# Kernel tuning notes

Measured on AMD Instinct MI355X. Metric: run time of the kernel, lower is better.

The kernel has to match this reference:

```python
import jax, jax.numpy as jnp
import numpy as np

B, S, D, E, TOPK = 8, 4096, 1024, 64, 2
TEMP = 0.01


def setup_inputs() -> dict:
    key = jax.random.key(0)
    k_x, k_w1, k_b1, k_w2, k_b2 = jax.random.split(key, 5)
    x = jax.random.normal(k_x, (B, S, D), dtype=jnp.float32)
    # torch.nn.Linear default init ~ U(-1/sqrt(fan_in), 1/sqrt(fan_in)); scale ok for reference
    W1 = jax.random.normal(k_w1, (D, 2 * D), dtype=jnp.float32) * (1.0 / np.sqrt(D))
    b1 = jax.random.normal(k_b1, (2 * D,), dtype=jnp.float32) * 0.01
    W2 = jax.random.normal(k_w2, (2 * D, E), dtype=jnp.float32) * (1.0 / np.sqrt(2 * D))
    b2 = jax.random.normal(k_b2, (E,), dtype=jnp.float32) * 0.01
    return {"x": x, "W1": W1, "b1": b1, "W2": W2, "b2": b2}


def reference(x, W1, b1, W2, b2):
    # 2-layer MLP router: [B,S,D] -> [B,S,2D] -> [B,S,E]
    h = jax.nn.relu(jnp.einsum('bsd,df->bsf', x, W1) + b1)
    logits = jnp.einsum('bsf,fe->bse', h, W2) + b2
    # top-k over experts
    top_k_logits, indices = jax.lax.top_k(logits, TOPK)  # [B,S,K]
    # scatter top-k logits into a -inf-filled tensor: equivalent to masking,
    # since scattered values equal logits at those positions
    keep = jax.nn.one_hot(indices, E, dtype=bool).any(axis=-2)  # [B,S,E]
    sparse_logits = jnp.where(keep, logits, -jnp.inf)
    router_output = jax.nn.softmax(sparse_logits, axis=-1)
    ori_router_output = jax.nn.softmax(logits / TEMP, axis=-1)
    return (ori_router_output, router_output, indices)
```

## Files before the change

### kernel.cpp

```cpp
#include <hip/hip_runtime.h>
#include <math.h>
#include <stdint.h>

#define M_TOK 32768
#define D_IN  1024
#define F_HID 2048
#define E_EXP 64

#define O_ORI 0
#define O_RTR (M_TOK * E_EXP)
#define O_IDX (2 * M_TOK * E_EXP)

typedef _Float16 half8 __attribute__((ext_vector_type(8)));
typedef float    f32x4 __attribute__((ext_vector_type(4)));
typedef unsigned int uint32;
typedef uint32   u32x4 __attribute__((ext_vector_type(4)));

#define WS_XH  ((size_t)0)
#define WS_XL  (WS_XH  + (size_t)M_TOK * D_IN * 2)
#define WS_W1H (WS_XL  + (size_t)M_TOK * D_IN * 2)
#define WS_W1L (WS_W1H + (size_t)D_IN * F_HID * 2)
#define WS_W2H (WS_W1L + (size_t)D_IN * F_HID * 2)
#define WS_W2L (WS_W2H + (size_t)F_HID * E_EXP * 2)
#define WS_H   (WS_W2L + (size_t)F_HID * E_EXP * 2)
#define WS_NEED_SPLIT (WS_H)
#define WS_NEED_FULL  (WS_H + (size_t)M_TOK * F_HID * 4)

__device__ __forceinline__ void split_sc(float v, float sc, unsigned short& h, unsigned short& l) {
    const _Float16 hh = (_Float16)v;
    const float hf = (float)hh;
    const _Float16 hs = (_Float16)(hf * sc);
    const _Float16 ls = (_Float16)((v - hf) * sc);
    h = __builtin_bit_cast(unsigned short, hs);
    l = __builtin_bit_cast(unsigned short, ls);
}


__global__ void split_x_k(const float* __restrict__ x,
                          unsigned short* __restrict__ xh, unsigned short* __restrict__ xl) {
    size_t i = ((size_t)blockIdx.x * 256 + threadIdx.x) * 4;
    const float4 v = *(const float4*)&x[i];
    ushort4 h, l;
    split_sc(v.x, 64.f, h.x, l.x); split_sc(v.y, 64.f, h.y, l.y);
    split_sc(v.z, 64.f, h.z, l.z); split_sc(v.w, 64.f, h.w, l.w);
    *(ushort4*)&xh[i] = h;
    *(ushort4*)&xl[i] = l;
}

__global__ void split_w1t_k(const float* __restrict__ W1,
                            unsigned short* __restrict__ wh, unsigned short* __restrict__ wl) {
    __shared__ float t[32][33];
    const int d0 = blockIdx.x * 32;
    const int f0 = blockIdx.y * 32;
    const int r  = threadIdx.x >> 3;
    const int c4 = (threadIdx.x & 7) * 4;
    const float4 v = *(const float4*)&W1[(size_t)(d0 + r) * F_HID + f0 + c4];
    t[r][c4 + 0] = v.x; t[r][c4 + 1] = v.y; t[r][c4 + 2] = v.z; t[r][c4 + 3] = v.w;
    __syncthreads();
    ushort4 h, l;
    split_sc(t[c4 + 0][r], 64.f, h.x, l.x);
    split_sc(t[c4 + 1][r], 64.f, h.y, l.y);
    split_sc(t[c4 + 2][r], 64.f, h.z, l.z);
    split_sc(t[c4 + 3][r], 64.f, h.w, l.w);
    *(ushort4*)&wh[(size_t)(f0 + r) * D_IN + d0 + c4] = h;
    *(ushort4*)&wl[(size_t)(f0 + r) * D_IN + d0 + c4] = l;
}

__global__ void split_w2t_k(const float* __restrict__ W2,
                            unsigned short* __restrict__ wh, unsigned short* __restrict__ wl) {
    const int gid = blockIdx.x * 256 + threadIdx.x;
    const int e  = gid >> 9;
    const int f4 = (gid & 511) * 4;
    ushort4 h, l;
    split_sc(W2[(size_t)(f4 + 0) * E_EXP + e], 16.f, h.x, l.x);
    split_sc(W2[(size_t)(f4 + 1) * E_EXP + e], 16.f, h.y, l.y);
    split_sc(W2[(size_t)(f4 + 2) * E_EXP + e], 16.f, h.z, l.z);
    split_sc(W2[(size_t)(f4 + 3) * E_EXP + e], 16.f, h.w, l.w);
    *(ushort4*)&wh[(size_t)e * F_HID + f4] = h;
    *(ushort4*)&wl[(size_t)e * F_HID + f4] = l;
}


__device__ __forceinline__ uint32 swz(uint32 o) { return o ^ (((o >> 7) & 7u) << 4); }

#define STAGE16(SRCP, DSTP) \
    __builtin_amdgcn_global_load_lds((const __attribute__((address_space(1))) void*)(SRCP), \
                                     (__attribute__((address_space(3))) void*)(DSTP), 16, 0, 0)


__launch_bounds__(512, 2)
__global__ void gemm1_8w(const unsigned short* __restrict__ xh, const unsigned short* __restrict__ xl,
                         const unsigned short* __restrict__ w1h, const unsigned short* __restrict__ w1l,
                         const float* __restrict__ b1,
                         uint32* __restrict__ hout)
{
    __shared__ __align__(16) unsigned char As[2][32768];
    __shared__ __align__(16) unsigned char Bs[2][32768];

    const int tid  = threadIdx.x;
    const int lane = tid & 63;
    const int w    = tid >> 6;
    const int c15  = lane & 15;
    const int g    = lane >> 4;
    const int wr   = w >> 2;
    const int wc   = w & 3;

    const int bid  = blockIdx.x;
    const int fblk = bid & 7;
    const int mblk = bid >> 3;
    const size_t tok0 = (size_t)mblk * 256;
    const int f0 = fblk * 256;

    uint32 srow[2], shalf[2];
#pragma unroll
    for (int j = 0; j < 2; ++j) {
        const uint32 c_ = (uint32)(w + 8 * j);
        const uint32 s_ = swz(c_ * 1024u + (uint32)lane * 16u);
        srow[j] = s_ >> 6; shalf[j] = (s_ & 63u) >> 1;
    }

    uint32 offA[8], offB[4];
#pragma unroll
    for (int m = 0; m < 8; ++m)
        offA[m] = swz((uint32)(wr * 128 + m * 16 + c15) * 64u + (uint32)g * 16u);
#pragma unroll
    for (int n = 0; n < 4; ++n)
        offB[n] = swz((uint32)(wc * 64 + n * 16 + c15) * 64u + (uint32)g * 16u);

    f32x4 acc[8][4];
#pragma unroll
    for (int m = 0; m < 8; ++m)
#pragma unroll
        for (int n = 0; n < 4; ++n) acc[m][n] = (f32x4){0.f, 0.f, 0.f, 0.f};

#define STAGE_T(T, BUF) do {                                                        \
    const int d0_ = (T) * 32;                                                       \
    _Pragma("unroll")                                                               \
    for (int j = 0; j < 2; ++j) {                                                   \
        const uint32 c_ = (uint32)(w + 8 * j);                                      \
        const size_t asrc = (tok0 + srow[j]) * D_IN + (size_t)(d0_ + (int)shalf[j]);\
        const size_t bsrc = ((size_t)(f0) + srow[j]) * D_IN + (size_t)(d0_ + (int)shalf[j]); \
        STAGE16(xh  + asrc, &As[BUF][c_ * 1024]);                                   \
        STAGE16(xl  + asrc, &As[BUF][16384 + c_ * 1024]);                           \
        STAGE16(w1h + bsrc, &Bs[BUF][c_ * 1024]);                                   \
        STAGE16(w1l + bsrc, &Bs[BUF][16384 + c_ * 1024]);                           \
    } } while (0)

    STAGE_T(0, 0);
    STAGE_T(1, 1);

#pragma unroll 1
    for (int t = 0; t < 32; ++t) {
        if (t < 31) asm volatile("s_waitcnt vmcnt(8)" ::: "memory");
        else        asm volatile("s_waitcnt vmcnt(0)" ::: "memory");
        __builtin_amdgcn_s_barrier();
        const unsigned char* Ab = As[t & 1];
        const unsigned char* Bb = Bs[t & 1];

        half8 b1f[4], b2f[4];
#pragma unroll
        for (int n = 0; n < 4; ++n) {
            b1f[n] = *(const half8*)(Bb + offB[n]);
            b2f[n] = *(const half8*)(Bb + 16384 + offB[n]);
        }
        half8 a1f[4], a2f[4];
#pragma unroll
        for (int m = 0; m < 4; ++m) {
            a1f[m] = *(const half8*)(Ab + offA[m]);
            a2f[m] = *(const half8*)(Ab + 16384 + offA[m]);
        }
        __builtin_amdgcn_s_setprio(1);
#pragma unroll
        for (int m = 0; m < 4; ++m)
#pragma unroll
            for (int n = 0; n < 4; ++n) {
                acc[m][n] = __builtin_amdgcn_mfma_f32_16x16x32_f16(a1f[m], b1f[n], acc[m][n], 0, 0, 0);
                acc[m][n] = __builtin_amdgcn_mfma_f32_16x16x32_f16(a1f[m], b2f[n], acc[m][n], 0, 0, 0);
                acc[m][n] = __builtin_amdgcn_mfma_f32_16x16x32_f16(a2f[m], b1f[n], acc[m][n], 0, 0, 0);
            }
        __builtin_amdgcn_s_setprio(0);
#pragma unroll
        for (int m = 0; m < 4; ++m) {
            a1f[m] = *(const half8*)(Ab + offA[4 + m]);
            a2f[m] = *(const half8*)(Ab + 16384 + offA[4 + m]);
        }
        __builtin_amdgcn_s_setprio(1);
#pragma unroll
        for (int m = 0; m < 4; ++m)
#pragma unroll
            for (int n = 0; n < 4; ++n) {
                acc[4 + m][n] = __builtin_amdgcn_mfma_f32_16x16x32_f16(a1f[m], b1f[n], acc[4 + m][n], 0, 0, 0);
                acc[4 + m][n] = __builtin_amdgcn_mfma_f32_16x16x32_f16(a1f[m], b2f[n], acc[4 + m][n], 0, 0, 0);
                acc[4 + m][n] = __builtin_amdgcn_mfma_f32_16x16x32_f16(a2f[m], b1f[n], acc[4 + m][n], 0, 0, 0);
            }
        __builtin_amdgcn_s_setprio(0);
        __builtin_amdgcn_s_barrier();
        if (t + 2 < 32) STAGE_T(t + 2, t & 1);
    }
#undef STAGE_T

    float bv[4];
#pragma unroll
    for (int n = 0; n < 4; ++n) bv[n] = b1[f0 + wc * 64 + n * 16 + c15];
#pragma unroll
    for (int m = 0; m < 8; ++m) {
        const size_t rowbase = (tok0 + (size_t)(wr * 128 + m * 16 + g * 4)) * F_HID;
#pragma unroll
        for (int n = 0; n < 4; ++n) {
            const int fcol = f0 + wc * 64 + n * 16 + c15;
#pragma unroll
            for (int r = 0; r < 4; ++r) {
                float hv = acc[m][n][r] * (1.f / 4096.f) + bv[n];
                hv = fmaxf(hv, 0.f);
                const _Float16 hh = (_Float16)hv;
                const float hf = (float)hh;
                const _Float16 hsv = (_Float16)(hf * 16.f);
                const _Float16 lsv = (_Float16)((hv - hf) * 16.f);
                const uint32 pk = (uint32)__builtin_bit_cast(unsigned short, hsv)
                                | ((uint32)__builtin_bit_cast(unsigned short, lsv) << 16);
                hout[rowbase + (size_t)r * F_HID + fcol] = pk;
            }
        }
    }
}


__launch_bounds__(256, 2)
__global__ void gemm2_epi(const uint32* __restrict__ hin,
                          const unsigned short* __restrict__ w2h, const unsigned short* __restrict__ w2l,
                          const float* __restrict__ b2,
                          float* __restrict__ out)
{
    __shared__ float ls[128 * 68];
    const int tid  = threadIdx.x;
    const int lane = tid & 63;
    const int w    = tid >> 6;
    const int c15  = lane & 15;
    const int g    = lane >> 4;
    const size_t tok0 = (size_t)blockIdx.x * 128;

    f32x4 acc[2][4];
#pragma unroll
    for (int mt = 0; mt < 2; ++mt)
#pragma unroll
        for (int nt = 0; nt < 4; ++nt) acc[mt][nt] = (f32x4){0.f, 0.f, 0.f, 0.f};

#pragma unroll 1
    for (int it = 0; it < 64; ++it) {
        const int fk = it * 32 + g * 8;
        half8 bf1[4], bf2[4];
#pragma unroll
        for (int nt = 0; nt < 4; ++nt) {
            const size_t eoff = (size_t)(nt * 16 + c15) * F_HID + fk;
            bf1[nt] = *(const half8*)&w2h[eoff];
            bf2[nt] = *(const half8*)&w2l[eoff];
        }
#pragma unroll
        for (int mt = 0; mt < 2; ++mt) {
            const uint32* hp = hin + (tok0 + (size_t)(w * 32 + mt * 16 + c15)) * F_HID + fk;
            const u32x4 q0 = *(const u32x4*)hp;
            const u32x4 q1 = *(const u32x4*)(hp + 4);
            u32x4 hi4, lo4;
            hi4[0] = __builtin_amdgcn_perm(q0[1], q0[0], 0x05040100u);
            hi4[1] = __builtin_amdgcn_perm(q0[3], q0[2], 0x05040100u);
            hi4[2] = __builtin_amdgcn_perm(q1[1], q1[0], 0x05040100u);
            hi4[3] = __builtin_amdgcn_perm(q1[3], q1[2], 0x05040100u);
            lo4[0] = __builtin_amdgcn_perm(q0[1], q0[0], 0x07060302u);
            lo4[1] = __builtin_amdgcn_perm(q0[3], q0[2], 0x07060302u);
            lo4[2] = __builtin_amdgcn_perm(q1[1], q1[0], 0x07060302u);
            lo4[3] = __builtin_amdgcn_perm(q1[3], q1[2], 0x07060302u);
            const half8 a1 = __builtin_bit_cast(half8, hi4);
            const half8 a2 = __builtin_bit_cast(half8, lo4);
#pragma unroll
            for (int nt = 0; nt < 4; ++nt) {
                acc[mt][nt] = __builtin_amdgcn_mfma_f32_16x16x32_f16(a1, bf1[nt], acc[mt][nt], 0, 0, 0);
                acc[mt][nt] = __builtin_amdgcn_mfma_f32_16x16x32_f16(a1, bf2[nt], acc[mt][nt], 0, 0, 0);
                acc[mt][nt] = __builtin_amdgcn_mfma_f32_16x16x32_f16(a2, bf1[nt], acc[mt][nt], 0, 0, 0);
            }
        }
    }

#pragma unroll
    for (int mt = 0; mt < 2; ++mt)
#pragma unroll
        for (int nt = 0; nt < 4; ++nt)
#pragma unroll
            for (int r = 0; r < 4; ++r)
                ls[(w * 32 + mt * 16 + g * 4 + r) * 68 + nt * 16 + c15] = acc[mt][nt][r] * (1.f / 256.f);
    __syncthreads();

    const int e = lane;
    const float be = b2[e];
#pragma unroll 1
    for (int i = 0; i < 32; ++i) {
        const float l = ls[(w * 32 + i) * 68 + e] + be;

        float v = l; int idx = e;
#pragma unroll
        for (int m = 32; m >= 1; m >>= 1) {
            const float ov = __shfl_xor(v, m, 64);
            const int   oi = __shfl_xor(idx, m, 64);
            if (ov > v || (ov == v && oi < idx)) { v = ov; idx = oi; }
        }
        const float m1 = v; const int i1 = idx;

        v = (e == i1) ? -INFINITY : l; idx = e;
#pragma unroll
        for (int m = 32; m >= 1; m >>= 1) {
            const float ov = __shfl_xor(v, m, 64);
            const int   oi = __shfl_xor(idx, m, 64);
            if (ov > v || (ov == v && oi < idx)) { v = ov; idx = oi; }
        }
        const int i2 = idx;

        const float ex = expf((l - m1) * 100.0f);
        float s = ex;
#pragma unroll
        for (int m = 32; m >= 1; m >>= 1) s += __shfl_xor(s, m, 64);
        const float ori = ex / s;

        const float q = (e == i1 || e == i2) ? expf(l - m1) : 0.f;
        float s2 = q;
#pragma unroll
        for (int m = 32; m >= 1; m >>= 1) s2 += __shfl_xor(s2, m, 64);
        const float rtr = q / s2;

        const size_t tok = tok0 + (size_t)w * 32 + i;
        out[O_ORI + tok * E_EXP + e] = ori;
        out[O_RTR + tok * E_EXP + e] = rtr;
        if (e == 0) {
            out[O_IDX + tok * 2 + 0] = (float)i1;
            out[O_IDX + tok * 2 + 1] = (float)i2;
        }
    }
}


#define BT  64
#define NB  256

__launch_bounds__(256, 2)
__global__ void router_mfma(const unsigned short* __restrict__ xh, const unsigned short* __restrict__ xl,
                            const unsigned short* __restrict__ w1h, const unsigned short* __restrict__ w1l,
                            const unsigned short* __restrict__ w2h, const unsigned short* __restrict__ w2l,
                            const float* __restrict__ b1, const float* __restrict__ b2,
                            float* __restrict__ out)
{
    __shared__ __align__(16) unsigned char xs_h[BT * 64];
    __shared__ __align__(16) unsigned char xs_l[BT * 64];
    __shared__ __align__(16) unsigned char w1s_h[NB * 64];
    __shared__ __align__(16) unsigned char w1s_l[NB * 64];
    __shared__ __align__(16) unsigned char hsbuf[BT * 132 * 4];

    const int tid  = threadIdx.x;
    const int lane = tid & 63;
    const int w    = tid >> 6;
    const int c15  = lane & 15;
    const int g    = lane >> 4;
    const size_t tok0 = (size_t)blockIdx.x * BT;

    uint32* hs = (uint32*)hsbuf;
    float*  ls = (float*)hsbuf;

    f32x4 acc2h[4], acc2x[4];
#pragma unroll
    for (int nt = 0; nt < 4; ++nt) {
        acc2h[nt] = (f32x4){0.f, 0.f, 0.f, 0.f};
        acc2x[nt] = (f32x4){0.f, 0.f, 0.f, 0.f};
    }

    const uint32 kqb = (uint32)g * 16u;

    for (int fc = 0; fc < F_HID; fc += NB) {
        f32x4 ahh[4][4], axx[4][4];
#pragma unroll
        for (int mt = 0; mt < 4; ++mt)
#pragma unroll
            for (int nt = 0; nt < 4; ++nt) {
                ahh[mt][nt] = (f32x4){0.f, 0.f, 0.f, 0.f};
                axx[mt][nt] = (f32x4){0.f, 0.f, 0.f, 0.f};
            }

        for (int d0 = 0; d0 < D_IN; d0 += 32) {
            __syncthreads();
            {
                uint32 o = (uint32)w * 1024u + (uint32)lane * 16u;
                uint32 s = swz(o);
                uint32 r = s >> 6, hb = (s & 63u) >> 1;
                const unsigned short* sp;
                sp = xh + (tok0 + r) * D_IN + (size_t)(d0 + (int)hb);
                STAGE16(sp, xs_h + (size_t)w * 1024);
                sp = xl + (tok0 + r) * D_IN + (size_t)(d0 + (int)hb);
                STAGE16(sp, xs_l + (size_t)w * 1024);
#pragma unroll
                for (int q = 0; q < 4; ++q) {
                    const uint32 c_ = (uint32)(q * 4 + w);
                    uint32 o2 = c_ * 1024u + (uint32)lane * 16u;
                    uint32 s2 = swz(o2);
                    uint32 r2 = s2 >> 6, hb2 = (s2 & 63u) >> 1;
                    sp = w1h + ((size_t)(fc + (int)r2)) * D_IN + (size_t)(d0 + (int)hb2);
                    STAGE16(sp, w1s_h + (size_t)c_ * 1024);
                    sp = w1l + ((size_t)(fc + (int)r2)) * D_IN + (size_t)(d0 + (int)hb2);
                    STAGE16(sp, w1s_l + (size_t)c_ * 1024);
                }
            }
            __syncthreads();

            half8 ah[4], al[4], bh[4], bl[4];
#pragma unroll
            for (int mt = 0; mt < 4; ++mt) {
                const uint32 off = swz((uint32)(mt * 16 + c15) * 64u + kqb);
                ah[mt] = *(const half8*)(xs_h + off);
                al[mt] = *(const half8*)(xs_l + off);
            }
#pragma unroll
            for (int nt = 0; nt < 4; ++nt) {
                const uint32 row = (uint32)(w * 64 + nt * 16 + c15);
                const uint32 off = swz(row * 64u + kqb);
                bh[nt] = *(const half8*)(w1s_h + off);
                bl[nt] = *(const half8*)(w1s_l + off);
            }
#pragma unroll
            for (int mt = 0; mt < 4; ++mt)
#pragma unroll
                for (int nt = 0; nt < 4; ++nt) {
                    ahh[mt][nt] = __builtin_amdgcn_mfma_f32_16x16x32_f16(ah[mt], bh[nt], ahh[mt][nt], 0, 0, 0);
                    axx[mt][nt] = __builtin_amdgcn_mfma_f32_16x16x32_f16(ah[mt], bl[nt], axx[mt][nt], 0, 0, 0);
                    axx[mt][nt] = __builtin_amdgcn_mfma_f32_16x16x32_f16(al[mt], bh[nt], axx[mt][nt], 0, 0, 0);
                }
        }

        const int fl0 = (w & 1) * 64;
#pragma unroll
        for (int phase = 0; phase < 2; ++phase) {
            if ((w >> 1) == phase) {
#pragma unroll
                for (int nt = 0; nt < 4; ++nt) {
                    const float b1v = b1[fc + w * 64 + nt * 16 + c15];
#pragma unroll
                    for (int mt = 0; mt < 4; ++mt) {
#pragma unroll
                        for (int r = 0; r < 4; ++r) {
                            float hv = (ahh[mt][nt][r] + axx[mt][nt][r]) * (1.f / 4096.f) + b1v;
                            hv = fmaxf(hv, 0.f);
                            const _Float16 hhv0 = (_Float16)hv;
                            const float hf = (float)hhv0;
                            const _Float16 hhv = (_Float16)(hf * 16.f);
                            const _Float16 hlv = (_Float16)((hv - hf) * 16.f);
                            uint32 pk = (uint32)__builtin_bit_cast(unsigned short, hhv)
                                      | ((uint32)__builtin_bit_cast(unsigned short, hlv) << 16);
                            const int t = mt * 16 + g * 4 + r;
                            hs[t * 132 + fl0 + nt * 16 + c15] = pk;
                        }
                    }
                }
            }
            __syncthreads();
            const int tA = w * 16 + c15;
#pragma unroll
            for (int ktl = 0; ktl < 4; ++ktl) {
                const u32x4 q0 = *(const u32x4*)&hs[tA * 132 + ktl * 32 + g * 8];
                const u32x4 q1 = *(const u32x4*)&hs[tA * 132 + ktl * 32 + g * 8 + 4];
                u32x4 hi4, lo4;
                hi4[0] = __builtin_amdgcn_perm(q0[1], q0[0], 0x05040100u);
                hi4[1] = __builtin_amdgcn_perm(q0[3], q0[2], 0x05040100u);
                hi4[2] = __builtin_amdgcn_perm(q1[1], q1[0], 0x05040100u);
                hi4[3] = __builtin_amdgcn_perm(q1[3], q1[2], 0x05040100u);
                lo4[0] = __builtin_amdgcn_perm(q0[1], q0[0], 0x07060302u);
                lo4[1] = __builtin_amdgcn_perm(q0[3], q0[2], 0x07060302u);
                lo4[2] = __builtin_amdgcn_perm(q1[1], q1[0], 0x07060302u);
                lo4[3] = __builtin_amdgcn_perm(q1[3], q1[2], 0x07060302u);
                const half8 a_h = __builtin_bit_cast(half8, hi4);
                const half8 a_l = __builtin_bit_cast(half8, lo4);
                const int fG = fc + (phase * 4 + ktl) * 32 + g * 8;
#pragma unroll
                for (int nt = 0; nt < 4; ++nt) {
                    const int e_ = nt * 16 + c15;
                    const half8 b_h = *(const half8*)&w2h[(size_t)e_ * F_HID + fG];
                    const half8 b_l = *(const half8*)&w2l[(size_t)e_ * F_HID + fG];
                    acc2h[nt] = __builtin_amdgcn_mfma_f32_16x16x32_f16(a_h, b_h, acc2h[nt], 0, 0, 0);
                    acc2x[nt] = __builtin_amdgcn_mfma_f32_16x16x32_f16(a_h, b_l, acc2x[nt], 0, 0, 0);
                    acc2x[nt] = __builtin_amdgcn_mfma_f32_16x16x32_f16(a_l, b_h, acc2x[nt], 0, 0, 0);
                }
            }
            __syncthreads();
        }
    }

#pragma unroll
    for (int nt = 0; nt < 4; ++nt)
#pragma unroll
        for (int r = 0; r < 4; ++r) {
            const int t = w * 16 + g * 4 + r;
            ls[t * 68 + nt * 16 + c15] = (acc2h[nt][r] + acc2x[nt][r]) * (1.f / 256.f);
        }
    __syncthreads();

    const int e = lane;
    const float be = b2[e];
#pragma unroll 1
    for (int i = 0; i < 16; ++i) {
        const float l = ls[(w * 16 + i) * 68 + e] + be;

        float v = l; int idx = e;
#pragma unroll
        for (int m = 32; m >= 1; m >>= 1) {
            const float ov = __shfl_xor(v, m, 64);
            const int   oi = __shfl_xor(idx, m, 64);
            if (ov > v || (ov == v && oi < idx)) { v = ov; idx = oi; }
        }
        const float m1 = v; const int i1 = idx;

        v = (e == i1) ? -INFINITY : l; idx = e;
#pragma unroll
        for (int m = 32; m >= 1; m >>= 1) {
            const float ov = __shfl_xor(v, m, 64);
            const int   oi = __shfl_xor(idx, m, 64);
            if (ov > v || (ov == v && oi < idx)) { v = ov; idx = oi; }
        }
        const int i2 = idx;

        const float ex = expf((l - m1) * 100.0f);
        float s = ex;
#pragma unroll
        for (int m = 32; m >= 1; m >>= 1) s += __shfl_xor(s, m, 64);
        const float ori = ex / s;

        const float q = (e == i1 || e == i2) ? expf(l - m1) : 0.f;
        float s2 = q;
#pragma unroll
        for (int m = 32; m >= 1; m >>= 1) s2 += __shfl_xor(s2, m, 64);
        const float rtr = q / s2;

        const size_t tok = tok0 + (size_t)w * 16 + i;
        out[O_ORI + tok * E_EXP + e] = ori;
        out[O_RTR + tok * E_EXP + e] = rtr;
        if (e == 0) {
            out[O_IDX + tok * 2 + 0] = (float)i1;
            out[O_IDX + tok * 2 + 1] = (float)i2;
        }
    }
}


extern "C" void kernel_launch(void* const* d_in, const int* in_sizes, int n_in,
                              void* d_out, int out_size, void* d_ws, size_t ws_size,
                              hipStream_t stream) {
    const float* x  = (const float*)d_in[0];
    const float* W1 = (const float*)d_in[1];
    const float* b1 = (const float*)d_in[2];
    const float* W2 = (const float*)d_in[3];
    const float* b2 = (const float*)d_in[4];
    float* out = (float*)d_out;

    unsigned char* ws = (unsigned char*)d_ws;
    unsigned short* xh  = (unsigned short*)(ws + WS_XH);
    unsigned short* xl  = (unsigned short*)(ws + WS_XL);
    unsigned short* w1h = (unsigned short*)(ws + WS_W1H);
    unsigned short* w1l = (unsigned short*)(ws + WS_W1L);
    unsigned short* w2h = (unsigned short*)(ws + WS_W2H);
    unsigned short* w2l = (unsigned short*)(ws + WS_W2L);
    uint32*         hbuf = (uint32*)(ws + WS_H);

    if (ws_size >= WS_NEED_FULL) {
        hipLaunchKernelGGL(split_x_k,  dim3(M_TOK * D_IN / 4 / 256), dim3(256), 0, stream, x, xh, xl);
        hipLaunchKernelGGL(split_w1t_k, dim3(D_IN / 32, F_HID / 32), dim3(256), 0, stream, W1, w1h, w1l);
        hipLaunchKernelGGL(split_w2t_k, dim3(F_HID * E_EXP / 4 / 256), dim3(256), 0, stream, W2, w2h, w2l);
        hipLaunchKernelGGL(gemm1_8w, dim3(1024), dim3(512), 0, stream, xh, xl, w1h, w1l, b1, hbuf);
        hipLaunchKernelGGL(gemm2_epi, dim3(M_TOK / 128), dim3(256), 0, stream, hbuf, w2h, w2l, b2, out);
    } else {
        hipLaunchKernelGGL(split_x_k,  dim3(M_TOK * D_IN / 4 / 256), dim3(256), 0, stream, x, xh, xl);
        hipLaunchKernelGGL(split_w1t_k, dim3(D_IN / 32, F_HID / 32), dim3(256), 0, stream, W1, w1h, w1l);
        hipLaunchKernelGGL(split_w2t_k, dim3(F_HID * E_EXP / 4 / 256), dim3(256), 0, stream, W2, w2h, w2l);
        hipLaunchKernelGGL(router_mfma, dim3(M_TOK / BT), dim3(256), 0, stream,
                           xh, xl, w1h, w1l, w2h, w2l, b1, b2, out);
    }
}
```

Measured before the change: 582.6 us.

## Fuse second GEMM into first via per-block split-K partials and finalize kernel

The hidden activation tensor (M×2D packed fp16 pairs) is no longer written to global memory. Each gemm1 block now stages its 256×256 hidden tile in LDS and multiplies it by the matching W2 slice, writing 8 split-K partial logit tensors that a new finalize kernel sums before top-k and softmax. This removes a large round trip of the hidden tensor through memory. In exchange it adds partial-sum traffic, LDS pressure that likely limits occupancy, and extra barriers. The main loop's A-fragment loads are also interleaved into four MFMA phases so the next tile's staging overlaps the last MFMA group.

```diff
diff --git a/kernel.cpp b/kernel.cpp
--- a/kernel.cpp
+++ b/kernel.cpp
@@ -22,9 +22,8 @@
 #define WS_W1L (WS_W1H + (size_t)D_IN * F_HID * 2)
 #define WS_W2H (WS_W1L + (size_t)D_IN * F_HID * 2)
 #define WS_W2L (WS_W2H + (size_t)F_HID * E_EXP * 2)
-#define WS_H   (WS_W2L + (size_t)F_HID * E_EXP * 2)
-#define WS_NEED_SPLIT (WS_H)
-#define WS_NEED_FULL  (WS_H + (size_t)M_TOK * F_HID * 4)
+#define WS_P   (WS_W2L + (size_t)F_HID * E_EXP * 2)
+#define WS_NEED_FULL (WS_P + (size_t)8 * M_TOK * E_EXP * 4)
 
 __device__ __forceinline__ void split_sc(float v, float sc, unsigned short& h, unsigned short& l) {
     const _Float16 hh = (_Float16)v;
@@ -82,6 +81,9 @@
 
 
 __device__ __forceinline__ uint32 swz(uint32 o) { return o ^ (((o >> 7) & 7u) << 4); }
+__device__ __forceinline__ uint32 hswz(int tok, int fl) {
+    return ((uint32)(tok * 512 + fl * 4)) ^ ((uint32)(tok & 7) << 4);
+}
 
 #define STAGE16(SRCP, DSTP) \
     __builtin_amdgcn_global_load_lds((const __attribute__((address_space(1))) void*)(SRCP), \
@@ -91,11 +93,11 @@
 __launch_bounds__(512, 2)
 __global__ void gemm1_8w(const unsigned short* __restrict__ xh, const unsigned short* __restrict__ xl,
                          const unsigned short* __restrict__ w1h, const unsigned short* __restrict__ w1l,
+                         const unsigned short* __restrict__ w2h, const unsigned short* __restrict__ w2l,
                          const float* __restrict__ b1,
-                         uint32* __restrict__ hout)
+                         float* __restrict__ partials)
 {
-    __shared__ __align__(16) unsigned char As[2][32768];
-    __shared__ __align__(16) unsigned char Bs[2][32768];
+    __shared__ __align__(16) unsigned char lds[131072];
 
     const int tid  = threadIdx.x;
     const int lane = tid & 63;
@@ -140,11 +142,21 @@
         const uint32 c_ = (uint32)(w + 8 * j);                                      \
         const size_t asrc = (tok0 + srow[j]) * D_IN + (size_t)(d0_ + (int)shalf[j]);\
         const size_t bsrc = ((size_t)(f0) + srow[j]) * D_IN + (size_t)(d0_ + (int)shalf[j]); \
-        STAGE16(xh  + asrc, &As[BUF][c_ * 1024]);                                   \
-        STAGE16(xl  + asrc, &As[BUF][16384 + c_ * 1024]);                           \
-        STAGE16(w1h + bsrc, &Bs[BUF][c_ * 1024]);                                   \
-        STAGE16(w1l + bsrc, &Bs[BUF][16384 + c_ * 1024]);                           \
+        STAGE16(xh  + asrc, lds + (BUF) * 32768 + c_ * 1024);                       \
+        STAGE16(xl  + asrc, lds + (BUF) * 32768 + 16384 + c_ * 1024);               \
+        STAGE16(w1h + bsrc, lds + 65536 + (BUF) * 32768 + c_ * 1024);               \
+        STAGE16(w1l + bsrc, lds + 65536 + (BUF) * 32768 + 16384 + c_ * 1024);       \
     } } while (0)
+
+#define MFMA_CL(MB, AH, AL)                                                          \
+    _Pragma("unroll")                                                                \
+    for (int mm = 0; mm < 2; ++mm)                                                   \
+        _Pragma("unroll")                                                            \
+        for (int n = 0; n < 4; ++n) {                                                \
+            acc[(MB)+mm][n] = __builtin_amdgcn_mfma_f32_16x16x32_f16((AH)[mm], b1f[n], acc[(MB)+mm][n], 0, 0, 0); \
+            acc[(MB)+mm][n] = __builtin_amdgcn_mfma_f32_16x16x32_f16((AH)[mm], b2f[n], acc[(MB)+mm][n], 0, 0, 0); \
+            acc[(MB)+mm][n] = __builtin_amdgcn_mfma_f32_16x16x32_f16((AL)[mm], b1f[n], acc[(MB)+mm][n], 0, 0, 0); \
+        }
 
     STAGE_T(0, 0);
     STAGE_T(1, 1);
@@ -154,146 +166,163 @@
         if (t < 31) asm volatile("s_waitcnt vmcnt(8)" ::: "memory");
         else        asm volatile("s_waitcnt vmcnt(0)" ::: "memory");
         __builtin_amdgcn_s_barrier();
-        const unsigned char* Ab = As[t & 1];
-        const unsigned char* Bb = Bs[t & 1];
-
-        half8 b1f[4], b2f[4];
+        const unsigned char* Ab = lds + (t & 1) * 32768;
+        const unsigned char* Bb = lds + 65536 + (t & 1) * 32768;
+
+        half8 b1f[4], b2f[4], aH0[2], aL0[2], aH1[2], aL1[2];
 #pragma unroll
         for (int n = 0; n < 4; ++n) {
             b1f[n] = *(const half8*)(Bb + offB[n]);
             b2f[n] = *(const half8*)(Bb + 16384 + offB[n]);
         }
-        half8 a1f[4], a2f[4];
-#pragma unroll
-        for (int m = 0; m < 4; ++m) {
-            a1f[m] = *(const half8*)(Ab + offA[m]);
-            a2f[m] = *(const half8*)(Ab + 16384 + offA[m]);
+#pragma unroll
+        for (int m = 0; m < 2; ++m) {
+            aH0[m] = *(const half8*)(Ab + offA[m]);
+            aL0[m] = *(const half8*)(Ab + 16384 + offA[m]);
         }
         __builtin_amdgcn_s_setprio(1);
-#pragma unroll
-        for (int m = 0; m < 4; ++m)
-#pragma unroll
-            for (int n = 0; n < 4; ++n) {
-                acc[m][n] = __builtin_amdgcn_mfma_f32_16x16x32_f16(a1f[m], b1f[n], acc[m][n], 0, 0, 0);
-                acc[m][n] = __builtin_amdgcn_mfma_f32_16x16x32_f16(a1f[m], b2f[n], acc[m][n], 0, 0, 0);
-                acc[m][n] = __builtin_amdgcn_mfma_f32_16x16x32_f16(a2f[m], b1f[n], acc[m][n], 0, 0, 0);
-            }
+        MFMA_CL(0, aH0, aL0)
         __builtin_amdgcn_s_setprio(0);
 #pragma unroll
-        for (int m = 0; m < 4; ++m) {
-            a1f[m] = *(const half8*)(Ab + offA[4 + m]);
-            a2f[m] = *(const half8*)(Ab + 16384 + offA[4 + m]);
-        }
+        for (int m = 0; m < 2; ++m) {
+            aH1[m] = *(const half8*)(Ab + offA[2 + m]);
+            aL1[m] = *(const half8*)(Ab + 16384 + offA[2 + m]);
+        }
+        __builtin_amdgcn_s_barrier();
         __builtin_amdgcn_s_setprio(1);
-#pragma unroll
-        for (int m = 0; m < 4; ++m)
-#pragma unroll
-            for (int n = 0; n < 4; ++n) {
-                acc[4 + m][n] = __builtin_amdgcn_mfma_f32_16x16x32_f16(a1f[m], b1f[n], acc[4 + m][n], 0, 0, 0);
-                acc[4 + m][n] = __builtin_amdgcn_mfma_f32_16x16x32_f16(a1f[m], b2f[n], acc[4 + m][n], 0, 0, 0);
-                acc[4 + m][n] = __builtin_amdgcn_mfma_f32_16x16x32_f16(a2f[m], b1f[n], acc[4 + m][n], 0, 0, 0);
-            }
+        MFMA_CL(2, aH1, aL1)
         __builtin_amdgcn_s_setprio(0);
+#pragma unroll
+        for (int m = 0; m < 2; ++m) {
+            aH0[m] = *(const half8*)(Ab + offA[4 + m]);
+            aL0[m] = *(const half8*)(Ab + 16384 + offA[4 + m]);
+        }
+        __builtin_amdgcn_s_barrier();
+        __builtin_amdgcn_s_setprio(1);
+        MFMA_CL(4, aH0, aL0)
+        __builtin_amdgcn_s_setprio(0);
+#pragma unroll
+        for (int m = 0; m < 2; ++m) {
+            aH1[m] = *(const half8*)(Ab + offA[6 + m]);
+            aL1[m] = *(const half8*)(Ab + 16384 + offA[6 + m]);
+        }
+        asm volatile("s_waitcnt lgkmcnt(0)" ::: "memory");
+        __builtin_amdgcn_sched_barrier(0);
         __builtin_amdgcn_s_barrier();
         if (t + 2 < 32) STAGE_T(t + 2, t & 1);
+        __builtin_amdgcn_s_setprio(1);
+        MFMA_CL(6, aH1, aL1)
+        __builtin_amdgcn_s_setprio(0);
     }
 #undef STAGE_T
 
+    uint32* hlds = (uint32*)lds;
+
     float bv[4];
 #pragma unroll
     for (int n = 0; n < 4; ++n) bv[n] = b1[f0 + wc * 64 + n * 16 + c15];
-#pragma unroll
-    for (int m = 0; m < 8; ++m) {
-        const size_t rowbase = (tok0 + (size_t)(wr * 128 + m * 16 + g * 4)) * F_HID;
-#pragma unroll
-        for (int n = 0; n < 4; ++n) {
-            const int fcol = f0 + wc * 64 + n * 16 + c15;
+
+    f32x4 acc2[2][4];
+#pragma unroll
+    for (int mt = 0; mt < 2; ++mt)
+#pragma unroll
+        for (int nt = 0; nt < 4; ++nt) acc2[mt][nt] = (f32x4){0.f, 0.f, 0.f, 0.f};
+
+    const int wtok0 = w * 32;
+
+#pragma unroll 1
+    for (int round = 0; round < 2; ++round) {
+        __builtin_amdgcn_s_barrier();
+        if ((wc >> 1) == round) {
+            const int flbase = (wc & 1) * 64;
+#pragma unroll
+            for (int m = 0; m < 8; ++m)
+#pragma unroll
+                for (int n = 0; n < 4; ++n)
+#pragma unroll
+                    for (int r = 0; r < 4; ++r) {
+                        float hv = acc[m][n][r] * (1.f / 4096.f) + bv[n];
+                        hv = fmaxf(hv, 0.f);
+                        const _Float16 hh = (_Float16)hv;
+                        const float hf = (float)hh;
+                        const _Float16 hsv = (_Float16)(hf * 16.f);
+                        const _Float16 lsv = (_Float16)((hv - hf) * 16.f);
+                        const uint32 pk = (uint32)__builtin_bit_cast(unsigned short, hsv)
+                                        | ((uint32)__builtin_bit_cast(unsigned short, lsv) << 16);
+                        const int tok = wr * 128 + m * 16 + g * 4 + r;
+                        const int fl  = flbase + n * 16 + c15;
+                        hlds[hswz(tok, fl) >> 2] = pk;
+                    }
+        }
+        __builtin_amdgcn_s_barrier();
+        const int fglob = f0 + round * 128;
+#pragma unroll
+        for (int ktl = 0; ktl < 4; ++ktl) {
+            const int kf = ktl * 32 + g * 8;
+            half8 bf1[4], bf2[4];
+#pragma unroll
+            for (int nt = 0; nt < 4; ++nt) {
+                const size_t eoff = (size_t)(nt * 16 + c15) * F_HID + fglob + kf;
+                bf1[nt] = *(const half8*)&w2h[eoff];
+                bf2[nt] = *(const half8*)&w2l[eoff];
+            }
+#pragma unroll
+            for (int mt = 0; mt < 2; ++mt) {
+                const int tok = wtok0 + mt * 16 + c15;
+                const u32x4 q0 = *(const u32x4*)((const unsigned char*)lds + hswz(tok, kf));
+                const u32x4 q1 = *(const u32x4*)((const unsigned char*)lds + hswz(tok, kf + 4));
+                u32x4 hi4, lo4;
+                hi4[0] = __builtin_amdgcn_perm(q0[1], q0[0], 0x05040100u);
+                hi4[1] = __builtin_amdgcn_perm(q0[3], q0[2], 0x05040100u);
+                hi4[2] = __builtin_amdgcn_perm(q1[1], q1[0], 0x05040100u);
+                hi4[3] = __builtin_amdgcn_perm(q1[3], q1[2], 0x05040100u);
+                lo4[0] = __builtin_amdgcn_perm(q0[1], q0[0], 0x07060302u);
+                lo4[1] = __builtin_amdgcn_perm(q0[3], q0[2], 0x07060302u);
+                lo4[2] = __builtin_amdgcn_perm(q1[1], q1[0], 0x07060302u);
+                lo4[3] = __builtin_amdgcn_perm(q1[3], q1[2], 0x07060302u);
+                const half8 a1 = __builtin_bit_cast(half8, hi4);
+                const half8 a2 = __builtin_bit_cast(half8, lo4);
+#pragma unroll
+                for (int nt = 0; nt < 4; ++nt) {
+                    acc2[mt][nt] = __builtin_amdgcn_mfma_f32_16x16x32_f16(a1, bf1[nt], acc2[mt][nt], 0, 0, 0);
+                    acc2[mt][nt] = __builtin_amdgcn_mfma_f32_16x16x32_f16(a1, bf2[nt], acc2[mt][nt], 0, 0, 0);
+                    acc2[mt][nt] = __builtin_amdgcn_mfma_f32_16x16x32_f16(a2, bf1[nt], acc2[mt][nt], 0, 0, 0);
+                }
+            }
+        }
+    }
+
+    float* pout = partials + ((size_t)fblk * M_TOK + tok0) * E_EXP;
+#pragma unroll
+    for (int mt = 0; mt < 2; ++mt)
+#pragma unroll
+        for (int nt = 0; nt < 4; ++nt)
 #pragma unroll
             for (int r = 0; r < 4; ++r) {
-                float hv = acc[m][n][r] * (1.f / 4096.f) + bv[n];
-                hv = fmaxf(hv, 0.f);
-                const _Float16 hh = (_Float16)hv;
-                const float hf = (float)hh;
-                const _Float16 hsv = (_Float16)(hf * 16.f);
-                const _Float16 lsv = (_Float16)((hv - hf) * 16.f);
-                const uint32 pk = (uint32)__builtin_bit_cast(unsigned short, hsv)
-                                | ((uint32)__builtin_bit_cast(unsigned short, lsv) << 16);
-                hout[rowbase + (size_t)r * F_HID + fcol] = pk;
-            }
-        }
-    }
-}
-
-
-__launch_bounds__(256, 2)
-__global__ void gemm2_epi(const uint32* __restrict__ hin,
-                          const unsigned short* __restrict__ w2h, const unsigned short* __restrict__ w2l,
-                          const float* __restrict__ b2,
-                          float* __restrict__ out)
+                const int tl = wtok0 + mt * 16 + g * 4 + r;
+                pout[(size_t)tl * E_EXP + nt * 16 + c15] = acc2[mt][nt][r] * (1.f / 256.f);
+            }
+}
+
+
+__launch_bounds__(256, 4)
+__global__ void finalize(const float* __restrict__ partials,
+                         const float* __restrict__ b2,
+                         float* __restrict__ out)
 {
-    __shared__ float ls[128 * 68];
-    const int tid  = threadIdx.x;
-    const int lane = tid & 63;
-    const int w    = tid >> 6;
-    const int c15  = lane & 15;
-    const int g    = lane >> 4;
-    const size_t tok0 = (size_t)blockIdx.x * 128;
-
-    f32x4 acc[2][4];
-#pragma unroll
-    for (int mt = 0; mt < 2; ++mt)
-#pragma unroll
-        for (int nt = 0; nt < 4; ++nt) acc[mt][nt] = (f32x4){0.f, 0.f, 0.f, 0.f};
-
-#pragma unroll 1
-    for (int it = 0; it < 64; ++it) {
-        const int fk = it * 32 + g * 8;
-        half8 bf1[4], bf2[4];
-#pragma unroll
-        for (int nt = 0; nt < 4; ++nt) {
-            const size_t eoff = (size_t)(nt * 16 + c15) * F_HID + fk;
-            bf1[nt] = *(const half8*)&w2h[eoff];
-            bf2[nt] = *(const half8*)&w2l[eoff];
-        }
-#pragma unroll
-        for (int mt = 0; mt < 2; ++mt) {
-            const uint32* hp = hin + (tok0 + (size_t)(w * 32 + mt * 16 + c15)) * F_HID + fk;
-            const u32x4 q0 = *(const u32x4*)hp;
-            const u32x4 q1 = *(const u32x4*)(hp + 4);
-            u32x4 hi4, lo4;
-            hi4[0] = __builtin_amdgcn_perm(q0[1], q0[0], 0x05040100u);
-            hi4[1] = __builtin_amdgcn_perm(q0[3], q0[2], 0x05040100u);
-            hi4[2] = __builtin_amdgcn_perm(q1[1], q1[0], 0x05040100u);
-            hi4[3] = __builtin_amdgcn_perm(q1[3], q1[2], 0x05040100u);
-            lo4[0] = __builtin_amdgcn_perm(q0[1], q0[0], 0x07060302u);
-            lo4[1] = __builtin_amdgcn_perm(q0[3], q0[2], 0x07060302u);
-            lo4[2] = __builtin_amdgcn_perm(q1[1], q1[0], 0x07060302u);
-            lo4[3] = __builtin_amdgcn_perm(q1[3], q1[2], 0x07060302u);
-            const half8 a1 = __builtin_bit_cast(half8, hi4);
-            const half8 a2 = __builtin_bit_cast(half8, lo4);
-#pragma unroll
-            for (int nt = 0; nt < 4; ++nt) {
-                acc[mt][nt] = __builtin_amdgcn_mfma_f32_16x16x32_f16(a1, bf1[nt], acc[mt][nt], 0, 0, 0);
-                acc[mt][nt] = __builtin_amdgcn_mfma_f32_16x16x32_f16(a1, bf2[nt], acc[mt][nt], 0, 0, 0);
-                acc[mt][nt] = __builtin_amdgcn_mfma_f32_16x16x32_f16(a2, bf1[nt], acc[mt][nt], 0, 0, 0);
-            }
-        }
-    }
-
-#pragma unroll
-    for (int mt = 0; mt < 2; ++mt)
-#pragma unroll
-        for (int nt = 0; nt < 4; ++nt)
-#pragma unroll
-            for (int r = 0; r < 4; ++r)
-                ls[(w * 32 + mt * 16 + g * 4 + r) * 68 + nt * 16 + c15] = acc[mt][nt][r] * (1.f / 256.f);
-    __syncthreads();
-
+    const int lane = threadIdx.x & 63;
+    const int w    = threadIdx.x >> 6;
+    const size_t tok0 = (size_t)blockIdx.x * 64;
     const int e = lane;
     const float be = b2[e];
+
 #pragma unroll 1
-    for (int i = 0; i < 32; ++i) {
-        const float l = ls[(w * 32 + i) * 68 + e] + be;
+    for (int i = 0; i < 16; ++i) {
+        const size_t tok = tok0 + (size_t)w * 16 + i;
+        float l = be;
+#pragma unroll
+        for (int p = 0; p < 8; ++p)
+            l += partials[((size_t)p * M_TOK + tok) * E_EXP + e];
 
         float v = l; int idx = e;
 #pragma unroll
@@ -325,7 +354,6 @@
         for (int m = 32; m >= 1; m >>= 1) s2 += __shfl_xor(s2, m, 64);
         const float rtr = q / s2;
 
-        const size_t tok = tok0 + (size_t)w * 32 + i;
         out[O_ORI + tok * E_EXP + e] = ori;
         out[O_RTR + tok * E_EXP + e] = rtr;
         if (e == 0) {
@@ -560,18 +588,17 @@
     unsigned short* w1l = (unsigned short*)(ws + WS_W1L);
     unsigned short* w2h = (unsigned short*)(ws + WS_W2H);
     unsigned short* w2l = (unsigned short*)(ws + WS_W2L);
-    uint32*         hbuf = (uint32*)(ws + WS_H);
+    float*          parts = (float*)(ws + WS_P);
+
+    hipLaunchKernelGGL(split_x_k,  dim3(M_TOK * D_IN / 4 / 256), dim3(256), 0, stream, x, xh, xl);
+    hipLaunchKernelGGL(split_w1t_k, dim3(D_IN / 32, F_HID / 32), dim3(256), 0, stream, W1, w1h, w1l);
+    hipLaunchKernelGGL(split_w2t_k, dim3(F_HID * E_EXP / 4 / 256), dim3(256), 0, stream, W2, w2h, w2l);
 
     if (ws_size >= WS_NEED_FULL) {
-        hipLaunchKernelGGL(split_x_k,  dim3(M_TOK * D_IN / 4 / 256), dim3(256), 0, stream, x, xh, xl);
-        hipLaunchKernelGGL(split_w1t_k, dim3(D_IN / 32, F_HID / 32), dim3(256), 0, stream, W1, w1h, w1l);
-        hipLaunchKernelGGL(split_w2t_k, dim3(F_HID * E_EXP / 4 / 256), dim3(256), 0, stream, W2, w2h, w2l);
-        hipLaunchKernelGGL(gemm1_8w, dim3(1024), dim3(512), 0, stream, xh, xl, w1h, w1l, b1, hbuf);
-        hipLaunchKernelGGL(gemm2_epi, dim3(M_TOK / 128), dim3(256), 0, stream, hbuf, w2h, w2l, b2, out);
+        hipLaunchKernelGGL(gemm1_8w, dim3(1024), dim3(512), 0, stream,
+                           xh, xl, w1h, w1l, w2h, w2l, b1, parts);
+        hipLaunchKernelGGL(finalize, dim3(M_TOK / 64), dim3(256), 0, stream, parts, b2, out);
     } else {
-        hipLaunchKernelGGL(split_x_k,  dim3(M_TOK * D_IN / 4 / 256), dim3(256), 0, stream, x, xh, xl);
-        hipLaunchKernelGGL(split_w1t_k, dim3(D_IN / 32, F_HID / 32), dim3(256), 0, stream, W1, w1h, w1l);
-        hipLaunchKernelGGL(split_w2t_k, dim3(F_HID * E_EXP / 4 / 256), dim3(256), 0, stream, W2, w2h, w2l);
         hipLaunchKernelGGL(router_mfma, dim3(M_TOK / BT), dim3(256), 0, stream,
                            xh, xl, w1h, w1l, w2h, w2l, b1, b2, out);
     }
```

Result: slower. 620.9 us (+6.6%).
